# Kernel optimization log

Hardware: AMD Instinct MI355X
Metric: run time of the kernel (lower is better)

## Reference

```python
import jax, jax.numpy as jnp
import numpy as np
import math

L, B, S, D, DK = 12, 2, 2048, 1024, 256
LN_EPS = 1e-5


def setup_inputs() -> dict:
    key = jax.random.key(0)
    k0, k1, k2 = jax.random.split(key, 3)
    states = jax.random.normal(k0, (L, B, S, D), dtype=jnp.float32)
    # nn.Linear default init ~ U(-1/sqrt(fan_in), 1/sqrt(fan_in))
    bound = 1.0 / math.sqrt(D)
    Wq = jax.random.uniform(k1, (DK, D), minval=-bound, maxval=bound, dtype=jnp.float32)
    Wk = jax.random.uniform(k2, (DK, D), minval=-bound, maxval=bound, dtype=jnp.float32)
    ln_weight = jnp.ones((D,), dtype=jnp.float32)
    ln_bias = jnp.zeros((D,), dtype=jnp.float32)
    latest_gate = jnp.asarray(0.5, dtype=jnp.float32)
    return {"states": states, "Wq": Wq, "Wk": Wk,
            "ln_weight": ln_weight, "ln_bias": ln_bias,
            "latest_gate": latest_gate}


def _layer_norm(x, w, b):
    mu = jnp.mean(x, axis=-1, keepdims=True)
    var = jnp.mean(jnp.square(x - mu), axis=-1, keepdims=True)
    return (x - mu) * jax.lax.rsqrt(var + LN_EPS) * w + b


def reference(states, Wq, Wk, ln_weight, ln_bias, latest_gate):
    # states: (L, B, S, D)
    normalized = _layer_norm(states, ln_weight, ln_bias)          # (L,B,S,D)
    latest = normalized[-1]                                       # (B,S,D)
    query = jnp.einsum('bsd,kd->bsk', latest, Wq)                 # (B,S,DK)
    keys = jnp.einsum('lbsd,kd->lbsk', normalized, Wk)            # (L,B,S,DK)
    scale = 1.0 / math.sqrt(query.shape[-1])
    logits = jnp.einsum('bsk,lbsk->lbs', query, keys) * scale     # (L,B,S)
    weights = jax.nn.softmax(logits, axis=0)                      # softmax over depth
    mixed = jnp.einsum('lbs,lbsd->bsd', weights, states)          # (B,S,D)
    gate = jax.nn.sigmoid(latest_gate)
    return gate * states[-1] + (1.0 - gate) * mixed
```

## Files before the change

### kernel.cpp

```cpp
#include <hip/hip_runtime.h>

#define NL 12
#define NB 2
#define NS 2048
#define ND 1024
#define NDK 256
#define NBS (NB*NS)

typedef __attribute__((ext_vector_type(8))) short short8;
typedef __attribute__((ext_vector_type(4))) short short4v;
typedef __attribute__((ext_vector_type(4))) float floatx4;

__device__ __forceinline__ unsigned short f2bf(float f) {
    unsigned int u = __float_as_uint(f);
    u += 0x7FFFu + ((u >> 16) & 1u);
    return (unsigned short)(u >> 16);
}
__device__ __forceinline__ short f2bfs(float f) { return (short)f2bf(f); }
__device__ __forceinline__ float bf2f(short s) {
    return __uint_as_float(((unsigned int)(unsigned short)s) << 16);
}

__global__ void k_prep_ln(const float* __restrict__ Wq, const float* __restrict__ Wk,
                          const float* __restrict__ x11,
                          const float* __restrict__ lnw, const float* __restrict__ lnb,
                          unsigned short* __restrict__ W2t, unsigned short* __restrict__ U) {
    const int tid = threadIdx.x;
    if (blockIdx.x < 256) {
        const int lane = tid & 63, wv = tid >> 6;
        const int wid = blockIdx.x * 4 + wv;
        const int tm = wid >> 4;
        const int tnb = wid & 15;
        const int lr = lane & 15, kh = lane >> 4;
        floatx4 acc[4];
#pragma unroll
        for (int c = 0; c < 4; ++c) acc[c] = (floatx4){0.f, 0.f, 0.f, 0.f};
#pragma unroll 2
        for (int kb = 0; kb < 8; ++kb) {
            const float* Ab = Wk + (size_t)(kb * 32 + kh * 8) * ND + tm * 16 + lr;
            const float* Bb = Wq + (size_t)(kb * 32 + kh * 8) * ND + tnb * 64 + lr;
            short8 a;
#pragma unroll
            for (int j = 0; j < 8; ++j) a[j] = f2bfs(Ab[(size_t)j * ND]);
#pragma unroll
            for (int c = 0; c < 4; ++c) {
                short8 b;
#pragma unroll
                for (int j = 0; j < 8; ++j) b[j] = f2bfs(Bb[(size_t)j * ND + c * 16]);
                acc[c] = __builtin_amdgcn_mfma_f32_16x16x32_bf16(a, b, acc[c], 0, 0, 0);
            }
        }
#pragma unroll
        for (int c = 0; c < 4; ++c)
#pragma unroll
            for (int r = 0; r < 4; ++r)
                W2t[(size_t)(tm * 16 + kh * 4 + r) * ND + tnb * 64 + c * 16 + lr] = f2bf(acc[c][r]);
        return;
    }
    __shared__ float red[8];
    const int p = blockIdx.x - 256;
    const float4* xr = (const float4*)(x11 + (size_t)p * ND);
    float4 x = xr[tid];
    float s1 = x.x + x.y + x.z + x.w;
    float s2 = x.x*x.x + x.y*x.y + x.z*x.z + x.w*x.w;
#pragma unroll
    for (int m = 32; m > 0; m >>= 1) { s1 += __shfl_xor(s1, m); s2 += __shfl_xor(s2, m); }
    int wv = tid >> 6;
    if ((tid & 63) == 0) { red[wv] = s1; red[4 + wv] = s2; }
    __syncthreads();
    float S1 = red[0] + red[1] + red[2] + red[3];
    float S2 = red[4] + red[5] + red[6] + red[7];
    float mu = S1 * (1.0f / ND);
    float var = S2 * (1.0f / ND) - mu * mu;
    float rstd = rsqrtf(var + 1e-5f);
    float4 w = ((const float4*)lnw)[tid];
    float4 b = ((const float4*)lnb)[tid];
    ushort4 u;
    u.x = f2bf((x.x - mu) * rstd * w.x + b.x);
    u.y = f2bf((x.y - mu) * rstd * w.y + b.y);
    u.z = f2bf((x.z - mu) * rstd * w.z + b.z);
    u.w = f2bf((x.w - mu) * rstd * w.w + b.w);
    ((ushort4*)U)[(size_t)p * (ND / 4) + tid] = u;
}

#define BM 64
#define BN 128
#define BK 64
#define LDP 72
__global__ __launch_bounds__(256) void k_vgemm(const unsigned short* __restrict__ U,
                                               const unsigned short* __restrict__ W2t,
                                               unsigned short* __restrict__ V) {
    __shared__ short8 AsV[(BM * LDP) / 8];
    __shared__ short8 BsV[(BN * LDP) / 8];
    unsigned short* As = (unsigned short*)AsV;
    unsigned short* Bs = (unsigned short*)BsV;
    const int tid = threadIdx.x;
    const int lane = tid & 63;
    const int wv = tid >> 6;
    const int wr = wv >> 1, wc = wv & 1;
    const int lr = lane & 15, kh = lane >> 4;
    const int bm0 = (blockIdx.x >> 3) * BM;
    const int bn0 = (blockIdx.x & 7) * BN;

    int aRow[2], aOff[2];
#pragma unroll
    for (int j = 0; j < 2; ++j) {
        int idx = j * 256 + tid;
        aRow[j] = idx >> 3;
        aOff[j] = (idx >> 3) * LDP + (idx & 7) * 8;
    }
    int bRow[4], bOff[4];
#pragma unroll
    for (int j = 0; j < 4; ++j) {
        int idx = j * 256 + tid;
        bRow[j] = idx >> 3;
        bOff[j] = (idx >> 3) * LDP + (idx & 7) * 8;
    }
    const short8* gA[2]; const short8* gB[4];
#pragma unroll
    for (int j = 0; j < 2; ++j)
        gA[j] = (const short8*)(U + (size_t)(bm0 + aRow[j]) * ND) + ((aOff[j] - aRow[j] * LDP) >> 3);
#pragma unroll
    for (int j = 0; j < 4; ++j)
        gB[j] = (const short8*)(W2t + (size_t)(bn0 + bRow[j]) * ND) + ((bOff[j] - bRow[j] * LDP) >> 3);

    floatx4 acc[2][4];
#pragma unroll
    for (int m = 0; m < 2; ++m)
#pragma unroll
        for (int n = 0; n < 4; ++n) acc[m][n] = (floatx4){0.f, 0.f, 0.f, 0.f};

    short8 ra[2], rb[4];
#pragma unroll
    for (int j = 0; j < 2; ++j) ra[j] = gA[j][0];
#pragma unroll
    for (int j = 0; j < 4; ++j) rb[j] = gB[j][0];

    const int NT = ND / BK;
#pragma unroll 1
    for (int t = 0; t < NT; ++t) {
        __syncthreads();
#pragma unroll
        for (int j = 0; j < 2; ++j) *(short8*)&As[aOff[j]] = ra[j];
#pragma unroll
        for (int j = 0; j < 4; ++j) *(short8*)&Bs[bOff[j]] = rb[j];
        __syncthreads();
        if (t < NT - 1) {
#pragma unroll
            for (int j = 0; j < 2; ++j) ra[j] = gA[j][(t + 1) * 8];
#pragma unroll
            for (int j = 0; j < 4; ++j) rb[j] = gB[j][(t + 1) * 8];
        }
#pragma unroll
        for (int kk = 0; kk < 2; ++kk) {
            short8 a[2], b[4];
#pragma unroll
            for (int m = 0; m < 2; ++m)
                a[m] = *(const short8*)&As[(wr * 32 + m * 16 + lr) * LDP + kk * 32 + kh * 8];
#pragma unroll
            for (int n = 0; n < 4; ++n)
                b[n] = *(const short8*)&Bs[(wc * 64 + n * 16 + lr) * LDP + kk * 32 + kh * 8];
#pragma unroll
            for (int m = 0; m < 2; ++m)
#pragma unroll
                for (int n = 0; n < 4; ++n)
                    acc[m][n] = __builtin_amdgcn_mfma_f32_16x16x32_bf16(a[m], b[n], acc[m][n], 0, 0, 0);
        }
    }
#pragma unroll
    for (int m = 0; m < 2; ++m)
#pragma unroll
        for (int n = 0; n < 4; ++n)
#pragma unroll
            for (int r = 0; r < 4; ++r)
                V[(size_t)(bm0 + wr * 32 + m * 16 + kh * 4 + r) * ND + bn0 + wc * 64 + n * 16 + lr]
                    = f2bf(acc[m][n][r]);
}

__global__ void k_fused(const float* __restrict__ states, const unsigned short* __restrict__ V,
                        const float* __restrict__ lnw, const float* __restrict__ lnb,
                        const float* __restrict__ gatep, float* __restrict__ out) {
    __shared__ float s_logit[12];
    __shared__ float s_w12[12];
    __shared__ float s_g;
    __shared__ float s_part[4][ND];
    __shared__ float s_x11[ND];
    const int p = blockIdx.x;
    const int tid = threadIdx.x;
    const int lane = tid & 63;
    const int wv = tid >> 6;
    const size_t LS = (size_t)NBS * ND;
    const float* base = states + (size_t)p * ND;
    const short4v* Vp = (const short4v*)(V + (size_t)p * ND);

    float4 t[4];
    float red[11];
#pragma unroll
    for (int j = 0; j < 11; ++j) red[j] = 0.f;
#pragma unroll
    for (int i = 0; i < 4; ++i) {
        int idx = lane + 64 * i;
        short4v vq = Vp[idx];
        float4 v;
        v.x = bf2f(vq[0]); v.y = bf2f(vq[1]); v.z = bf2f(vq[2]); v.w = bf2f(vq[3]);
        float4 w = ((const float4*)lnw)[idx];
        float4 b = ((const float4*)lnb)[idx];
        float4 tt; tt.x = v.x*w.x; tt.y = v.y*w.y; tt.z = v.z*w.z; tt.w = v.w*w.w;
        t[i] = tt;
        red[9]  += tt.x + tt.y + tt.z + tt.w;
        red[10] += v.x*b.x + v.y*b.y + v.z*b.z + v.w*b.w;
    }

    float4 x[3][4];
#pragma unroll
    for (int rr = 0; rr < 3; ++rr) {
        const int l = wv + 4 * rr;
        const float4* xr = (const float4*)(base + (size_t)l * LS);
#pragma unroll
        for (int i = 0; i < 4; ++i) {
            float4 xx = xr[lane + 64 * i];
            x[rr][i] = xx;
            red[rr]     += xx.x + xx.y + xx.z + xx.w;
            red[3 + rr] += xx.x*xx.x + xx.y*xx.y + xx.z*xx.z + xx.w*xx.w;
            red[6 + rr] += xx.x*t[i].x + xx.y*t[i].y + xx.z*t[i].z + xx.w*t[i].w;
        }
    }
#pragma unroll
    for (int m = 32; m > 0; m >>= 1) {
#pragma unroll
        for (int j = 0; j < 11; ++j) red[j] += __shfl_xor(red[j], m);
    }
    if (lane == 0) {
#pragma unroll
        for (int rr = 0; rr < 3; ++rr) {
            float mu = red[rr] * (1.0f / ND);
            float var = red[3 + rr] * (1.0f / ND) - mu * mu;
            float rstd = rsqrtf(var + 1e-5f);
            s_logit[wv + 4 * rr] = 0.0625f * (rstd * (red[6 + rr] - mu * red[9]) + red[10]);
        }
    }
    __syncthreads();
    if (tid == 0) {
        float mx = s_logit[0];
#pragma unroll
        for (int l = 1; l < 12; ++l) mx = fmaxf(mx, s_logit[l]);
        float e[12], sum = 0.f;
#pragma unroll
        for (int l = 0; l < 12; ++l) { e[l] = expf(s_logit[l] - mx); sum += e[l]; }
        float inv = 1.0f / sum;
#pragma unroll
        for (int l = 0; l < 12; ++l) s_w12[l] = e[l] * inv;
        s_g = 1.0f / (1.0f + expf(-gatep[0]));
    }
    __syncthreads();

    const float w0 = s_w12[wv], w1 = s_w12[wv + 4], w2 = s_w12[wv + 8];
#pragma unroll
    for (int i = 0; i < 4; ++i) {
        int idx = lane + 64 * i;
        float4 pm;
        pm.x = w0*x[0][i].x + w1*x[1][i].x + w2*x[2][i].x;
        pm.y = w0*x[0][i].y + w1*x[1][i].y + w2*x[2][i].y;
        pm.z = w0*x[0][i].z + w1*x[1][i].z + w2*x[2][i].z;
        pm.w = w0*x[0][i].w + w1*x[1][i].w + w2*x[2][i].w;
        ((float4*)s_part[wv])[idx] = pm;
        if (wv == 3) ((float4*)s_x11)[idx] = x[2][i];
    }
    __syncthreads();

    const float g = s_g;
    float4 a0 = ((const float4*)s_part[0])[tid];
    float4 a1 = ((const float4*)s_part[1])[tid];
    float4 a2 = ((const float4*)s_part[2])[tid];
    float4 a3 = ((const float4*)s_part[3])[tid];
    float4 x11 = ((const float4*)s_x11)[tid];
    float4 o;
    o.x = g * x11.x + (1.f - g) * (a0.x + a1.x + a2.x + a3.x);
    o.y = g * x11.y + (1.f - g) * (a0.y + a1.y + a2.y + a3.y);
    o.z = g * x11.z + (1.f - g) * (a0.z + a1.z + a2.z + a3.z);
    o.w = g * x11.w + (1.f - g) * (a0.w + a1.w + a2.w + a3.w);
    ((float4*)(out + (size_t)p * ND))[tid] = o;
}

extern "C" void kernel_launch(void* const* d_in, const int* in_sizes, int n_in,
                              void* d_out, int out_size, void* d_ws, size_t ws_size,
                              hipStream_t stream) {
    (void)in_sizes; (void)n_in; (void)out_size; (void)ws_size;
    const float* states = (const float*)d_in[0];
    const float* Wq     = (const float*)d_in[1];
    const float* Wk     = (const float*)d_in[2];
    const float* lnw    = (const float*)d_in[3];
    const float* lnb    = (const float*)d_in[4];
    const float* gate   = (const float*)d_in[5];
    float* out = (float*)d_out;
    char* ws = (char*)d_ws;

    unsigned short* U   = (unsigned short*)(ws);
    unsigned short* W2t = (unsigned short*)(ws + (9u << 20));
    unsigned short* V   = (unsigned short*)(ws + (12u << 20));

    k_prep_ln<<<dim3(256 + NBS), dim3(256), 0, stream>>>(
        Wq, Wk, states + (size_t)(NL - 1) * NBS * ND, lnw, lnb, W2t, U);
    k_vgemm<<<dim3((NBS / BM) * (ND / BN)), dim3(256), 0, stream>>>(U, W2t, V);
    k_fused<<<dim3(NBS), dim3(256), 0, stream>>>(states, V, lnw, lnb, gate, out);
}
```

Measured before the change: 75.43 us.

## Double-buffer GEMM shared tiles and stage output through LDS for coalesced stores

```diff
diff --git a/kernel.cpp b/kernel.cpp
--- a/kernel.cpp
+++ b/kernel.cpp
@@ -87,13 +87,12 @@
 #define BN 128
 #define BK 64
 #define LDP 72
+#define TLP 132
 __global__ __launch_bounds__(256) void k_vgemm(const unsigned short* __restrict__ U,
                                                const unsigned short* __restrict__ W2t,
                                                unsigned short* __restrict__ V) {
-    __shared__ short8 AsV[(BM * LDP) / 8];
-    __shared__ short8 BsV[(BN * LDP) / 8];
-    unsigned short* As = (unsigned short*)AsV;
-    unsigned short* Bs = (unsigned short*)BsV;
+    __shared__ unsigned short As[2][BM * LDP];
+    __shared__ unsigned short Bs[2][BN * LDP];
     const int tid = threadIdx.x;
     const int lane = tid & 63;
     const int wv = tid >> 6;
@@ -102,27 +101,23 @@
     const int bm0 = (blockIdx.x >> 3) * BM;
     const int bn0 = (blockIdx.x & 7) * BN;
 
-    int aRow[2], aOff[2];
+    int aOff[2], bOff[4];
+    const short8* gA[2];
+    const short8* gB[4];
 #pragma unroll
     for (int j = 0; j < 2; ++j) {
         int idx = j * 256 + tid;
-        aRow[j] = idx >> 3;
-        aOff[j] = (idx >> 3) * LDP + (idx & 7) * 8;
-    }
-    int bRow[4], bOff[4];
+        int row = idx >> 3, c8 = idx & 7;
+        aOff[j] = row * LDP + c8 * 8;
+        gA[j] = (const short8*)(U + (size_t)(bm0 + row) * ND) + c8;
+    }
 #pragma unroll
     for (int j = 0; j < 4; ++j) {
         int idx = j * 256 + tid;
-        bRow[j] = idx >> 3;
-        bOff[j] = (idx >> 3) * LDP + (idx & 7) * 8;
-    }
-    const short8* gA[2]; const short8* gB[4];
-#pragma unroll
-    for (int j = 0; j < 2; ++j)
-        gA[j] = (const short8*)(U + (size_t)(bm0 + aRow[j]) * ND) + ((aOff[j] - aRow[j] * LDP) >> 3);
-#pragma unroll
-    for (int j = 0; j < 4; ++j)
-        gB[j] = (const short8*)(W2t + (size_t)(bn0 + bRow[j]) * ND) + ((bOff[j] - bRow[j] * LDP) >> 3);
+        int row = idx >> 3, c8 = idx & 7;
+        bOff[j] = row * LDP + c8 * 8;
+        gB[j] = (const short8*)(W2t + (size_t)(bn0 + row) * ND) + c8;
+    }
 
     floatx4 acc[2][4];
 #pragma unroll
@@ -139,11 +134,12 @@
     const int NT = ND / BK;
 #pragma unroll 1
     for (int t = 0; t < NT; ++t) {
-        __syncthreads();
-#pragma unroll
-        for (int j = 0; j < 2; ++j) *(short8*)&As[aOff[j]] = ra[j];
-#pragma unroll
-        for (int j = 0; j < 4; ++j) *(short8*)&Bs[bOff[j]] = rb[j];
+        unsigned short* Ab = As[t & 1];
+        unsigned short* Bb = Bs[t & 1];
+#pragma unroll
+        for (int j = 0; j < 2; ++j) *(short8*)&Ab[aOff[j]] = ra[j];
+#pragma unroll
+        for (int j = 0; j < 4; ++j) *(short8*)&Bb[bOff[j]] = rb[j];
         __syncthreads();
         if (t < NT - 1) {
 #pragma unroll
@@ -156,10 +152,10 @@
             short8 a[2], b[4];
 #pragma unroll
             for (int m = 0; m < 2; ++m)
-                a[m] = *(const short8*)&As[(wr * 32 + m * 16 + lr) * LDP + kk * 32 + kh * 8];
+                a[m] = *(const short8*)&Ab[(wr * 32 + m * 16 + lr) * LDP + kk * 32 + kh * 8];
 #pragma unroll
             for (int n = 0; n < 4; ++n)
-                b[n] = *(const short8*)&Bs[(wc * 64 + n * 16 + lr) * LDP + kk * 32 + kh * 8];
+                b[n] = *(const short8*)&Bb[(wc * 64 + n * 16 + lr) * LDP + kk * 32 + kh * 8];
 #pragma unroll
             for (int m = 0; m < 2; ++m)
 #pragma unroll
@@ -167,14 +163,23 @@
                     acc[m][n] = __builtin_amdgcn_mfma_f32_16x16x32_bf16(a[m], b[n], acc[m][n], 0, 0, 0);
         }
     }
+
+    __syncthreads();
+    unsigned short* Cs = (unsigned short*)As;
 #pragma unroll
     for (int m = 0; m < 2; ++m)
 #pragma unroll
         for (int n = 0; n < 4; ++n)
 #pragma unroll
             for (int r = 0; r < 4; ++r)
-                V[(size_t)(bm0 + wr * 32 + m * 16 + kh * 4 + r) * ND + bn0 + wc * 64 + n * 16 + lr]
-                    = f2bf(acc[m][n][r]);
+                Cs[(wr * 32 + m * 16 + kh * 4 + r) * TLP + wc * 64 + n * 16 + lr] = f2bf(acc[m][n][r]);
+    __syncthreads();
+#pragma unroll
+    for (int j = 0; j < 4; ++j) {
+        int idx = j * 256 + tid;
+        int row = idx >> 4, c8 = idx & 15;
+        *(short8*)&V[(size_t)(bm0 + row) * ND + bn0 + c8 * 8] = *(const short8*)&Cs[row * TLP + c8 * 8];
+    }
 }
 
 __global__ void k_fused(const float* __restrict__ states, const unsigned short* __restrict__ V,
```

Result: no change. 74.84 us (-0.8%).
